# Performance work log

Measured on AMD Instinct MI355X. Metric: run time of the kernel, lower is better.

The kernel has to match this reference:

```python
import jax, jax.numpy as jnp
import numpy as np

B, N, K, D = 8, 32768, 128, 64
TAU, ITERS, EPS = 1.0, 10, 1e-8


def setup_inputs() -> dict:
    key = jax.random.key(0)
    k1, k2, k3 = jax.random.split(key, 3)
    xyz = jax.random.normal(k1, (B, 3, N), dtype=jnp.float32)
    feats = jax.random.normal(k2, (B, D, N), dtype=jnp.float32)
    o_scores = jax.random.uniform(k3, (B, N), dtype=jnp.float32)
    return {"xyz": xyz, "feats": feats, "o_scores": o_scores}


def _sq_dist(x, c):
    # x: (B,N,3), c: (B,K,3) -> (B,N,K) squared euclidean distance
    x2 = jnp.sum(x * x, axis=-1, keepdims=True)          # (B,N,1)
    c2 = jnp.sum(c * c, axis=-1)[:, None, :]              # (B,1,K)
    xc = jnp.einsum('bnd,bkd->bnk', x, c)                 # (B,N,K)
    return x2 + c2 - 2.0 * xc


def _wkeans_plus(x, f, s, n_clusters, iters, tau):
    # x: (B,N,3) points, f: (B,N,D) features, s: (B,N) soft weights
    n = x.shape[1]
    # deterministic init: evenly strided points as initial centroids
    init_idx = jnp.arange(n_clusters) * (n // n_clusters)
    centers = x[:, init_idx, :]                           # (B,K,3)
    w = s[..., None]                                      # (B,N,1)
    s_sum = jnp.sum(s, axis=1, keepdims=True) + EPS       # (B,1)
    gamma = None
    denom = None
    for _ in range(iters):
        d = _sq_dist(x, centers)                          # (B,N,K)
        gamma = jax.nn.softmax(-d / tau, axis=-1) * w     # (B,N,K) weighted soft assignment
        denom = jnp.sum(gamma, axis=1) + EPS              # (B,K)
        centers = jnp.einsum('bnk,bnd->bkd', gamma, x) / denom[..., None]
    pi = jnp.sum(gamma, axis=1) / s_sum                   # (B,K) mixing weights
    node_feats = jnp.einsum('bnk,bnd->bkd', gamma, f) / denom[..., None]  # (B,K,D)
    return gamma, pi, centers, node_feats


def reference(xyz, feats, o_scores):
    x = jnp.swapaxes(xyz, -1, -2)    # (B,N,3)
    f = jnp.swapaxes(feats, -1, -2)  # (B,N,D)
    gamma, pi, node_xyz, node_feats = _wkeans_plus(x, f, o_scores, K, ITERS, TAU)
    return gamma, pi, node_xyz, node_feats
```

## Files before the change

kernel.cpp:

```cpp
#include <hip/hip_runtime.h>

#define BB 8
#define NN 32768
#define KK 128
#define DD 64
#define TAU 1.0f
#define ITERS 10
#define EPSV 1e-8f
#define JPARTS 128

#define G_SZ   ((size_t)BB * NN * KK)
#define PI_OFF (G_SZ)
#define XY_OFF (PI_OFF + (size_t)BB * KK)
#define NF_OUT (XY_OFF + (size_t)BB * KK * 3)

#define SLICE_F (BB * KK * 4)
#define SS_OFF  ((ITERS + 1) * SLICE_F)
#define HDR_F   (SS_OFF + 16)
#define PART_OFF HDR_F
#define PART_F  ((size_t)JPARTS * BB * KK * DD)
#define WS_NEED_BYTES ((PART_OFF + PART_F) * 4)

__global__ __launch_bounds__(256) void prep_kernel(const float* __restrict__ xyz,
                                                   const float* __restrict__ sc,
                                                   float* __restrict__ ws) {
    int b = blockIdx.x, tid = threadIdx.x, wave = tid >> 6, lane = tid & 63;
    const float* S = sc + (size_t)b * NN;
    float sum = 0.f;
    for (int i = tid; i < NN; i += 256) sum += S[i];
    #pragma unroll
    for (int m = 1; m <= 32; m <<= 1) sum += __shfl_xor(sum, m, 64);
    __shared__ float red[4];
    if (lane == 0) red[wave] = sum;
    __syncthreads();
    if (tid == 0) ws[SS_OFF + b] = red[0] + red[1] + red[2] + red[3] + EPSV;
    if (tid < KK) {
        const float* X = xyz + (size_t)b * 3 * NN;
        int i0 = tid * (NN / KK);
        ((float4*)ws)[b * KK + tid] =
            make_float4(X[i0], X[NN + i0], X[2 * NN + i0], 1.0f);
    }
}

template <bool LAST>
__global__ __launch_bounds__(256) void assign_kernel(
    const float* __restrict__ xyz, const float* __restrict__ sc,
    const float4* __restrict__ accIn,
    float* __restrict__ accOut,
    float* __restrict__ gamma_out)
{
    __shared__ float4 cLds[KK];
    __shared__ float4 wLds[256];
    __shared__ float  accW[4][512];

    const int b = blockIdx.y, blk = blockIdx.x;
    const int tid = threadIdx.x, wave = tid >> 6, lane = tid & 63;

    const float* X = xyz + (size_t)b * 3 * NN;
    const float* S = sc + (size_t)b * NN;

    const int n = blk * 256 + tid;
    const float px = X[n], py = X[NN + n], pz = X[2 * NN + n], ps = S[n];

    if (tid < KK) {
        float4 a = accIn[b * KK + tid];
        float denom = a.w + EPSV;
        float cx = a.x / denom, cy = a.y / denom, cz = a.z / denom;
        cLds[tid] = make_float4(2.f * cx / TAU, 2.f * cy / TAU, 2.f * cz / TAU,
                                -(cx * cx + cy * cy + cz * cz) / TAU);
    }
    __syncthreads();

    float l0 = 0.f, l1 = 0.f;
    #pragma unroll 8
    for (int k = 0; k < KK; k += 2) {
        float4 ca = cLds[k], cb = cLds[k + 1];
        l0 += __expf(fmaf(px, ca.x, fmaf(py, ca.y, fmaf(pz, ca.z, ca.w))));
        l1 += __expf(fmaf(px, cb.x, fmaf(py, cb.y, fmaf(pz, cb.z, cb.w))));
    }
    wLds[tid] = make_float4(px, py, pz, ps / (l0 + l1));
    __syncthreads();

    const float4 c0 = cLds[lane];
    const float4 c1 = cLds[lane + 64];
    float ax0 = 0, ay0 = 0, az0 = 0, aw0 = 0;
    float ax1 = 0, ay1 = 0, az1 = 0, aw1 = 0;
    float* grow = gamma_out + ((size_t)b * NN + blk * 256 + (wave << 6)) * KK + lane;

    #pragma unroll 4
    for (int j = 0; j < 64; ++j) {
        float4 P = wLds[(wave << 6) | j];
        float g0 = __expf(fmaf(P.x, c0.x, fmaf(P.y, c0.y, fmaf(P.z, c0.z, c0.w)))) * P.w;
        float g1 = __expf(fmaf(P.x, c1.x, fmaf(P.y, c1.y, fmaf(P.z, c1.z, c1.w)))) * P.w;
        if (LAST) {
            grow[(size_t)j * KK] = g0;
            grow[(size_t)j * KK + 64] = g1;
        }
        ax0 = fmaf(g0, P.x, ax0); ay0 = fmaf(g0, P.y, ay0);
        az0 = fmaf(g0, P.z, az0); aw0 += g0;
        ax1 = fmaf(g1, P.x, ax1); ay1 = fmaf(g1, P.y, ay1);
        az1 = fmaf(g1, P.z, az1); aw1 += g1;
    }

    ((float4*)accW[wave])[lane]      = make_float4(ax0, ay0, az0, aw0);
    ((float4*)accW[wave])[lane + 64] = make_float4(ax1, ay1, az1, aw1);
    __syncthreads();
    float v0 = accW[0][tid]       + accW[1][tid]       + accW[2][tid]       + accW[3][tid];
    float v1 = accW[0][tid + 256] + accW[1][tid + 256] + accW[2][tid + 256] + accW[3][tid + 256];
    float* ag = accOut + b * (KK * 4);
    atomicAdd(ag + tid, v0);
    atomicAdd(ag + tid + 256, v1);
}

__global__ void final_kernel(const float* __restrict__ ws, float* __restrict__ out) {
    int b = blockIdx.x, k = threadIdx.x;
    float4 a = ((const float4*)(ws + ITERS * SLICE_F))[b * KK + k];
    float denom = a.w + EPSV;
    float* oxyz = out + XY_OFF + (size_t)(b * KK + k) * 3;
    oxyz[0] = a.x / denom; oxyz[1] = a.y / denom; oxyz[2] = a.z / denom;
    out[PI_OFF + b * KK + k] = a.w / ws[SS_OFF + b];
}

template <bool ATOMIC>
__global__ __launch_bounds__(256) void nf_compute(const float* __restrict__ gamma,
                                                  const float* __restrict__ feats,
                                                  float* __restrict__ dst) {
    __shared__ float gLds[32 * 128];
    __shared__ float fLds[64 * 33];
    const int b = blockIdx.y, part = blockIdx.x, tid = threadIdx.x;
    const int kq = (tid & 15) * 8, dg = (tid >> 4) * 4;

    float acc[8][4];
    #pragma unroll
    for (int i = 0; i < 8; i++)
        #pragma unroll
        for (int u = 0; u < 4; u++) acc[i][u] = 0.f;

    const float* gb = gamma + (size_t)b * NN * KK + (size_t)part * (NN / JPARTS) * KK;
    const float* fb = feats + (size_t)b * DD * NN + part * (NN / JPARTS);

    for (int ch = 0; ch < (NN / JPARTS) / 32; ++ch) {
        const float4* gs = (const float4*)(gb + (size_t)ch * 32 * KK);
        #pragma unroll
        for (int i = 0; i < 4; i++) ((float4*)gLds)[tid + i * 256] = gs[tid + i * 256];
        #pragma unroll
        for (int i = 0; i < 2; i++) {
            int idx = tid + i * 256;
            int d = idx >> 3, c4 = (idx & 7) * 4;
            float4 fv = *(const float4*)(fb + (size_t)d * NN + ch * 32 + c4);
            float* fr = &fLds[d * 33 + c4];
            fr[0] = fv.x; fr[1] = fv.y; fr[2] = fv.z; fr[3] = fv.w;
        }
        __syncthreads();
        #pragma unroll 4
        for (int nl = 0; nl < 32; ++nl) {
            float4 g0 = *(const float4*)&gLds[nl * 128 + kq];
            float4 g1 = *(const float4*)&gLds[nl * 128 + kq + 4];
            float fv[4];
            #pragma unroll
            for (int u = 0; u < 4; u++) fv[u] = fLds[(dg + u) * 33 + nl];
            float gk[8] = {g0.x, g0.y, g0.z, g0.w, g1.x, g1.y, g1.z, g1.w};
            #pragma unroll
            for (int i = 0; i < 8; i++)
                #pragma unroll
                for (int u = 0; u < 4; u++)
                    acc[i][u] = fmaf(gk[i], fv[u], acc[i][u]);
        }
        __syncthreads();
    }

    if (ATOMIC) {
        float* nf = dst + (size_t)b * KK * DD;
        #pragma unroll
        for (int i = 0; i < 8; i++)
            #pragma unroll
            for (int u = 0; u < 4; u++)
                atomicAdd(&nf[(kq + i) * DD + dg + u], acc[i][u]);
    } else {
        float* p = dst + ((size_t)(b * JPARTS + part)) * (KK * DD);
        #pragma unroll
        for (int i = 0; i < 8; i++)
            *(float4*)&p[(kq + i) * DD + dg] =
                make_float4(acc[i][0], acc[i][1], acc[i][2], acc[i][3]);
    }
}

__global__ __launch_bounds__(256) void nf_reduce(const float* __restrict__ ws,
                                                 float* __restrict__ out) {
    int idx = blockIdx.x * 256 + threadIdx.x;
    int b = idx >> 13, e = idx & 8191;
    const float* p = ws + PART_OFF + (size_t)b * JPARTS * (KK * DD) + e;
    float sum = 0.f;
    #pragma unroll 8
    for (int j = 0; j < JPARTS; ++j) sum += p[(size_t)j * (KK * DD)];
    int k = e >> 6;
    float denom = ws[ITERS * SLICE_F + (b * KK + k) * 4 + 3] + EPSV;
    out[NF_OUT + idx] = sum / denom;
}

__global__ __launch_bounds__(256) void nf_finalize(const float* __restrict__ ws,
                                                   float* __restrict__ out) {
    int idx = blockIdx.x * 256 + threadIdx.x;
    int bk = idx / DD;
    float denom = ws[ITERS * SLICE_F + bk * 4 + 3] + EPSV;
    out[NF_OUT + idx] = out[NF_OUT + idx] / denom;
}

extern "C" void kernel_launch(void* const* d_in, const int* in_sizes, int n_in,
                              void* d_out, int out_size, void* d_ws, size_t ws_size,
                              hipStream_t stream) {
    const float* xyz = (const float*)d_in[0];
    const float* feats = (const float*)d_in[1];
    const float* sc = (const float*)d_in[2];
    float* out = (float*)d_out;
    float* ws = (float*)d_ws;

    hipMemsetAsync(ws, 0, (size_t)HDR_F * sizeof(float), stream);
    prep_kernel<<<BB, 256, 0, stream>>>(xyz, sc, ws);

    for (int it = 0; it < ITERS - 1; it++) {
        assign_kernel<false><<<dim3(128, BB), 256, 0, stream>>>(
            xyz, sc, (const float4*)(ws + it * SLICE_F),
            ws + (it + 1) * SLICE_F, out);
    }
    assign_kernel<true><<<dim3(128, BB), 256, 0, stream>>>(
        xyz, sc, (const float4*)(ws + (ITERS - 1) * SLICE_F),
        ws + ITERS * SLICE_F, out);

    final_kernel<<<BB, KK, 0, stream>>>(ws, out);

    if (ws_size >= WS_NEED_BYTES) {
        nf_compute<false><<<dim3(JPARTS, BB), 256, 0, stream>>>(out, feats, ws + PART_OFF);
        nf_reduce<<<256, 256, 0, stream>>>(ws, out);
    } else {
        hipMemsetAsync(out + NF_OUT, 0, (size_t)BB * KK * DD * sizeof(float), stream);
        nf_compute<true><<<dim3(JPARTS, BB), 256, 0, stream>>>(out, feats, out + NF_OUT);
        nf_finalize<<<256, 256, 0, stream>>>(ws, out);
    }
}
```

Before: 330.0 us.

## Compute node features with bf16 MFMA from a transposed gamma copy

The final assignment pass also writes a transposed, bf16-packed copy of gamma into the workspace. A new nf_mfma kernel reads that copy together with feats converted to bf16 and computes the per-part gamma^T·feats products with 16x16x32 bf16 MFMA instructions instead of scalar FMA through LDS. This replaces a reload of the full fp32 gamma with a half-size read and matrix-core throughput. The costs are extra writes in the last assign pass, reduced precision in node_feats, and a large workspace requirement that decides whether the path runs.

```diff
diff --git a/kernel.cpp b/kernel.cpp
--- a/kernel.cpp
+++ b/kernel.cpp
@@ -1,4 +1,8 @@
 #include <hip/hip_runtime.h>
+#include <hip/hip_bf16.h>
+
+typedef __attribute__((ext_vector_type(8))) short short8;
+typedef __attribute__((ext_vector_type(4))) float f32x4;
 
 #define BB 8
 #define NN 32768
@@ -19,7 +23,14 @@
 #define HDR_F   (SS_OFF + 16)
 #define PART_OFF HDR_F
 #define PART_F  ((size_t)JPARTS * BB * KK * DD)
-#define WS_NEED_BYTES ((PART_OFF + PART_F) * 4)
+#define GT_OFF  (PART_OFF + PART_F)
+#define WS_NEED_BYTES  ((PART_OFF + PART_F) * 4)
+#define WS_MFMA_BYTES  ((GT_OFF + (size_t)BB * KK * NN / 2) * 4)
+
+__device__ __forceinline__ unsigned pk2(float a, float b) {
+    __hip_bfloat162 h = __float22bfloat162_rn(make_float2(a, b));
+    unsigned u; __builtin_memcpy(&u, &h, 4); return u;
+}
 
 __global__ __launch_bounds__(256) void prep_kernel(const float* __restrict__ xyz,
                                                    const float* __restrict__ sc,
@@ -45,9 +56,8 @@
 template <bool LAST>
 __global__ __launch_bounds__(256) void assign_kernel(
     const float* __restrict__ xyz, const float* __restrict__ sc,
-    const float4* __restrict__ accIn,
-    float* __restrict__ accOut,
-    float* __restrict__ gamma_out)
+    const float4* __restrict__ accIn, float* __restrict__ accOut,
+    float* __restrict__ gamma_out, unsigned short* __restrict__ gt)
 {
     __shared__ float4 cLds[KK];
     __shared__ float4 wLds[256];
@@ -87,19 +97,42 @@
     float ax1 = 0, ay1 = 0, az1 = 0, aw1 = 0;
     float* grow = gamma_out + ((size_t)b * NN + blk * 256 + (wave << 6)) * KK + lane;
 
-    #pragma unroll 4
-    for (int j = 0; j < 64; ++j) {
-        float4 P = wLds[(wave << 6) | j];
-        float g0 = __expf(fmaf(P.x, c0.x, fmaf(P.y, c0.y, fmaf(P.z, c0.z, c0.w)))) * P.w;
-        float g1 = __expf(fmaf(P.x, c1.x, fmaf(P.y, c1.y, fmaf(P.z, c1.z, c1.w)))) * P.w;
+    unsigned* r0 = nullptr; unsigned* r1 = nullptr;
+    if (LAST) {
+        int n0w = blk * 256 + (wave << 6);
+        r0 = (unsigned*)gt + ((size_t)b * KK + lane) * (NN / 2) + n0w / 2;
+        r1 = r0 + (size_t)64 * (NN / 2);
+    }
+    unsigned pk0[4], pk1[4];
+
+    #pragma unroll
+    for (int jp = 0; jp < 32; ++jp) {
+        float4 Pa = wLds[(wave << 6) | (2 * jp)];
+        float4 Pb = wLds[(wave << 6) | (2 * jp + 1)];
+        float g0a = __expf(fmaf(Pa.x, c0.x, fmaf(Pa.y, c0.y, fmaf(Pa.z, c0.z, c0.w)))) * Pa.w;
+        float g1a = __expf(fmaf(Pa.x, c1.x, fmaf(Pa.y, c1.y, fmaf(Pa.z, c1.z, c1.w)))) * Pa.w;
+        float g0b = __expf(fmaf(Pb.x, c0.x, fmaf(Pb.y, c0.y, fmaf(Pb.z, c0.z, c0.w)))) * Pb.w;
+        float g1b = __expf(fmaf(Pb.x, c1.x, fmaf(Pb.y, c1.y, fmaf(Pb.z, c1.z, c1.w)))) * Pb.w;
         if (LAST) {
-            grow[(size_t)j * KK] = g0;
-            grow[(size_t)j * KK + 64] = g1;
-        }
-        ax0 = fmaf(g0, P.x, ax0); ay0 = fmaf(g0, P.y, ay0);
-        az0 = fmaf(g0, P.z, az0); aw0 += g0;
-        ax1 = fmaf(g1, P.x, ax1); ay1 = fmaf(g1, P.y, ay1);
-        az1 = fmaf(g1, P.z, az1); aw1 += g1;
+            grow[(size_t)(2 * jp) * KK] = g0a;
+            grow[(size_t)(2 * jp) * KK + 64] = g1a;
+            grow[(size_t)(2 * jp + 1) * KK] = g0b;
+            grow[(size_t)(2 * jp + 1) * KK + 64] = g1b;
+            pk0[jp & 3] = pk2(g0a, g0b);
+            pk1[jp & 3] = pk2(g1a, g1b);
+            if ((jp & 3) == 3 && gt) {
+                ((uint4*)r0)[jp >> 2] = make_uint4(pk0[0], pk0[1], pk0[2], pk0[3]);
+                ((uint4*)r1)[jp >> 2] = make_uint4(pk1[0], pk1[1], pk1[2], pk1[3]);
+            }
+        }
+        ax0 = fmaf(g0a, Pa.x, ax0); ay0 = fmaf(g0a, Pa.y, ay0);
+        az0 = fmaf(g0a, Pa.z, az0); aw0 += g0a;
+        ax1 = fmaf(g1a, Pa.x, ax1); ay1 = fmaf(g1a, Pa.y, ay1);
+        az1 = fmaf(g1a, Pa.z, az1); aw1 += g1a;
+        ax0 = fmaf(g0b, Pb.x, ax0); ay0 = fmaf(g0b, Pb.y, ay0);
+        az0 = fmaf(g0b, Pb.z, az0); aw0 += g0b;
+        ax1 = fmaf(g1b, Pb.x, ax1); ay1 = fmaf(g1b, Pb.y, ay1);
+        az1 = fmaf(g1b, Pb.z, az1); aw1 += g1b;
     }
 
     ((float4*)accW[wave])[lane]      = make_float4(ax0, ay0, az0, aw0);
@@ -121,6 +154,53 @@
     out[PI_OFF + b * KK + k] = a.w / ws[SS_OFF + b];
 }
 
+__global__ __launch_bounds__(256) void nf_mfma(const unsigned short* __restrict__ gt,
+                                               const float* __restrict__ feats,
+                                               float* __restrict__ dst) {
+    const int b = blockIdx.y, part = blockIdx.x;
+    const int tid = threadIdx.x, wave = tid >> 6, lane = tid & 63;
+    const int r = lane & 15, hi = lane >> 4;
+
+    f32x4 acc[2][4];
+    #pragma unroll
+    for (int kt = 0; kt < 2; kt++)
+        #pragma unroll
+        for (int dt = 0; dt < 4; dt++) acc[kt][dt] = (f32x4){0.f, 0.f, 0.f, 0.f};
+
+    const unsigned short* gtb = gt + ((size_t)b * KK + wave * 32 + r) * NN;
+    const float* fb = feats + (size_t)b * DD * NN;
+    const int n0 = part * (NN / JPARTS);
+
+    for (int ch = 0; ch < (NN / JPARTS) / 32; ++ch) {
+        const int nn = n0 + ch * 32 + hi * 8;
+        short8 a0 = *(const short8*)(gtb + nn);
+        short8 a1 = *(const short8*)(gtb + (size_t)16 * NN + nn);
+        union { unsigned u[4]; short8 s; } bu[4];
+        #pragma unroll
+        for (int dt = 0; dt < 4; dt++) {
+            const float* fr = fb + (size_t)(dt * 16 + r) * NN + nn;
+            float4 x = *(const float4*)fr;
+            float4 y = *(const float4*)(fr + 4);
+            bu[dt].u[0] = pk2(x.x, x.y); bu[dt].u[1] = pk2(x.z, x.w);
+            bu[dt].u[2] = pk2(y.x, y.y); bu[dt].u[3] = pk2(y.z, y.w);
+        }
+        #pragma unroll
+        for (int dt = 0; dt < 4; dt++) {
+            acc[0][dt] = __builtin_amdgcn_mfma_f32_16x16x32_bf16(a0, bu[dt].s, acc[0][dt], 0, 0, 0);
+            acc[1][dt] = __builtin_amdgcn_mfma_f32_16x16x32_bf16(a1, bu[dt].s, acc[1][dt], 0, 0, 0);
+        }
+    }
+
+    float* p = dst + ((size_t)(b * JPARTS + part)) * (KK * DD) + (size_t)(wave * 32) * DD;
+    #pragma unroll
+    for (int kt = 0; kt < 2; kt++)
+        #pragma unroll
+        for (int dt = 0; dt < 4; dt++)
+            #pragma unroll
+            for (int rr = 0; rr < 4; rr++)
+                p[(kt * 16 + hi * 4 + rr) * DD + dt * 16 + r] = acc[kt][dt][rr];
+}
+
 template <bool ATOMIC>
 __global__ __launch_bounds__(256) void nf_compute(const float* __restrict__ gamma,
                                                   const float* __restrict__ feats,
@@ -129,16 +209,13 @@
     __shared__ float fLds[64 * 33];
     const int b = blockIdx.y, part = blockIdx.x, tid = threadIdx.x;
     const int kq = (tid & 15) * 8, dg = (tid >> 4) * 4;
-
     float acc[8][4];
     #pragma unroll
     for (int i = 0; i < 8; i++)
         #pragma unroll
         for (int u = 0; u < 4; u++) acc[i][u] = 0.f;
-
     const float* gb = gamma + (size_t)b * NN * KK + (size_t)part * (NN / JPARTS) * KK;
     const float* fb = feats + (size_t)b * DD * NN + part * (NN / JPARTS);
-
     for (int ch = 0; ch < (NN / JPARTS) / 32; ++ch) {
         const float4* gs = (const float4*)(gb + (size_t)ch * 32 * KK);
         #pragma unroll
@@ -168,7 +245,6 @@
         }
         __syncthreads();
     }
-
     if (ATOMIC) {
         float* nf = dst + (size_t)b * KK * DD;
         #pragma unroll
@@ -215,21 +291,27 @@
     float* out = (float*)d_out;
     float* ws = (float*)d_ws;
 
+    const bool mfma_path = ws_size >= WS_MFMA_BYTES;
+    unsigned short* gt = mfma_path ? (unsigned short*)(ws + GT_OFF) : nullptr;
+
     hipMemsetAsync(ws, 0, (size_t)HDR_F * sizeof(float), stream);
     prep_kernel<<<BB, 256, 0, stream>>>(xyz, sc, ws);
 
     for (int it = 0; it < ITERS - 1; it++) {
         assign_kernel<false><<<dim3(128, BB), 256, 0, stream>>>(
             xyz, sc, (const float4*)(ws + it * SLICE_F),
-            ws + (it + 1) * SLICE_F, out);
+            ws + (it + 1) * SLICE_F, out, nullptr);
     }
     assign_kernel<true><<<dim3(128, BB), 256, 0, stream>>>(
         xyz, sc, (const float4*)(ws + (ITERS - 1) * SLICE_F),
-        ws + ITERS * SLICE_F, out);
+        ws + ITERS * SLICE_F, out, gt);
 
     final_kernel<<<BB, KK, 0, stream>>>(ws, out);
 
-    if (ws_size >= WS_NEED_BYTES) {
+    if (mfma_path) {
+        nf_mfma<<<dim3(JPARTS, BB), 256, 0, stream>>>(gt, feats, ws + PART_OFF);
+        nf_reduce<<<256, 256, 0, stream>>>(ws, out);
+    } else if (ws_size >= WS_NEED_BYTES) {
         nf_compute<false><<<dim3(JPARTS, BB), 256, 0, stream>>>(out, feats, ws + PART_OFF);
         nf_reduce<<<256, 256, 0, stream>>>(ws, out);
     } else {
```

Result: slower. 340.3 us (+3.1%).
